# Kernel optimization log

Hardware: AMD Instinct MI355X
Metric: run time of the kernel (lower is better)

## Reference

```python
import jax, jax.numpy as jnp
import numpy as np

LAMBDA_MAX = 2.0  # standard re-scaled Laplacian assumption (DGL lambda_max=[2])
NUM_GRAPHS = 100


def _cheb(feat, src, dst, d_invsqrt, W, b):
    # DGL ChebConv: h = sum_i fc_i(X_i) + b, X_i = Chebyshev recursion on scaled Laplacian
    n = feat.shape[0]
    k = W.shape[0]
    re = 2.0 / LAMBDA_MAX

    def aggr(f):  # D^{-1/2} A D^{-1/2} f  via gather + segment_sum
        fh = f * d_invsqrt
        m = jax.ops.segment_sum(fh[src], dst, num_segments=n)
        return m * d_invsqrt

    X0 = feat
    h = X0 @ W[0]
    if k > 1:
        X1 = -re * aggr(X0) + X0 * (re - 1.0)
        h = h + X1 @ W[1]
        for i in range(2, k):
            Xi = -2.0 * re * aggr(X1) + X1 * (2.0 * (re - 1.0)) - X0
            h = h + Xi @ W[i]
            X0, X1 = X1, Xi
    return h + b


def _edgeconv(feat, src, dst, Wt, bt, Wp, bp):
    # DGL EdgeConv: out_i = max_{j->i} [theta(x_i - x_j) + phi(x_i)], 0 if no in-edges
    n = feat.shape[0]
    theta = (feat[dst] - feat[src]) @ Wt + bt           # [E, H]
    phi = feat @ Wp + bp                                # [N, H]
    msg = theta + phi[dst]                              # [E, H]
    agg = jax.ops.segment_max(msg, dst, num_segments=n)
    return jnp.where(jnp.isfinite(agg), agg, jnp.zeros((), feat.dtype))


def setup_inputs() -> dict:
    key = jax.random.key(0)
    ks = jax.random.split(key, 20)
    N, E, G = 100000, 1600000, NUM_GRAPHS
    IN, H, K = 16, 64, 3

    def lin(k, fan_in, shape):
        return jax.random.normal(k, shape, dtype=jnp.float32) * (1.0 / np.sqrt(fan_in))

    inp = {}
    inp["feat"] = jax.random.normal(ks[0], (N, IN), dtype=jnp.float32)
    inp["src"] = jax.random.randint(ks[1], (E,), 0, N)
    inp["dst"] = jax.random.randint(ks[2], (E,), 0, N)
    inp["graph_ids"] = jnp.sort(jax.random.randint(ks[3], (N,), 0, G))
    # ChebConv params: W [k, in, out], b [out]
    inp["W1"] = lin(ks[4], IN, (K, IN, H)); inp["b1"] = jnp.zeros((H,), jnp.float32)
    inp["W2"] = lin(ks[5], H, (K, H, H));   inp["b2"] = jnp.zeros((H,), jnp.float32)
    inp["W3"] = lin(ks[6], H, (K, H, H));   inp["b3"] = jnp.zeros((H,), jnp.float32)
    # EdgeConv params: theta + phi linears
    inp["Wt1"] = lin(ks[7], H, (H, H));  inp["bt1"] = jnp.zeros((H,), jnp.float32)
    inp["Wp1"] = lin(ks[8], H, (H, H));  inp["bp1"] = jnp.zeros((H,), jnp.float32)
    inp["Wt2"] = lin(ks[9], H, (H, H));  inp["bt2"] = jnp.zeros((H,), jnp.float32)
    inp["Wp2"] = lin(ks[10], H, (H, H)); inp["bp2"] = jnp.zeros((H,), jnp.float32)
    return inp


def reference(feat, src, dst, graph_ids, W1, b1, W2, b2, W3, b3,
              Wt1, bt1, Wp1, bp1, Wt2, bt2, Wp2, bp2):
    n = feat.shape[0]
    deg = jax.ops.segment_sum(jnp.ones((src.shape[0],), feat.dtype), dst, num_segments=n)
    d_invsqrt = (jnp.clip(deg, 1.0, None) ** -0.5)[:, None]  # [N, 1]

    h = jax.nn.relu(_cheb(feat, src, dst, d_invsqrt, W1, b1))
    h = jax.nn.relu(_edgeconv(h, src, dst, Wt1, bt1, Wp1, bp1))
    h = jax.nn.relu(_cheb(h, src, dst, d_invsqrt, W2, b2))
    h = jax.nn.relu(_edgeconv(h, src, dst, Wt2, bt2, Wp2, bp2))
    h = jax.nn.relu(_cheb(h, src, dst, d_invsqrt, W3, b3))

    # dgl.mean_nodes: per-graph mean pooling
    counts = jax.ops.segment_sum(jnp.ones((n,), h.dtype), graph_ids, num_segments=NUM_GRAPHS)
    hg = jax.ops.segment_sum(h, graph_ids, num_segments=NUM_GRAPHS)
    return hg / jnp.clip(counts, 1.0, None)[:, None]
```

## Files before the change

### kernel.cpp

```cpp
#include <hip/hip_runtime.h>
#include <hip/hip_bf16.h>
#include <math.h>

typedef __attribute__((ext_vector_type(8))) short short8;
typedef __attribute__((ext_vector_type(4))) float floatx4;

__device__ __forceinline__ unsigned short bfb(float x) {
    union { __hip_bfloat16 h; unsigned short u; } c;
    c.h = __float2bfloat16(x);
    return c.u;
}
__device__ __forceinline__ float bf2f(unsigned short u) {
    union { unsigned int i; float f; } c;
    c.i = ((unsigned int)u) << 16;
    return c.f;
}
__device__ __forceinline__ void acc2(float& lo, float& hi, unsigned d) {
    union { unsigned u; float f; } a, b;
    a.u = d << 16;
    b.u = d & 0xffff0000u;
    lo += a.f; hi += b.f;
}
__device__ __forceinline__ unsigned pkmaxu16(unsigned a, unsigned b) {
    unsigned d;
    asm("v_pk_max_u16 %0, %1, %2" : "=v"(d) : "v"(a), "v"(b));
    return d;
}


__global__ __launch_bounds__(256) void k_bhist(const int* __restrict__ dst, int* __restrict__ bcnt, int E) {
    __shared__ int h[512];
    int t = threadIdx.x;
    for (int i = t; i < 512; i += 256) h[i] = 0;
    __syncthreads();
    int step = gridDim.x * 256;
    for (int i = blockIdx.x * 256 + t; i < E; i += step) atomicAdd(&h[dst[i] >> 8], 1);
    __syncthreads();
    for (int i = t; i < 512; i += 256) if (h[i]) atomicAdd(&bcnt[i], h[i]);
}

__global__ __launch_bounds__(512) void k_scanBkt(const int* __restrict__ bcnt, int* __restrict__ boff,
                                                 int* __restrict__ bcur, int nb, int E) {
    __shared__ int s[512];
    int t = threadIdx.x;
    int v = (t < nb) ? bcnt[t] : 0;
    s[t] = v;
    __syncthreads();
    for (int off = 1; off < 512; off <<= 1) {
        int x = (t >= off) ? s[t - off] : 0;
        __syncthreads();
        s[t] += x;
        __syncthreads();
    }
    if (t < nb) { boff[t] = s[t] - v; bcur[t] = s[t] - v; }
    if (t == 0) boff[nb] = E;
}

#define PCHUNK 8192

__global__ __launch_bounds__(256) void k_partA(const int* __restrict__ src, const int* __restrict__ dst,
                                               int* __restrict__ bcur, unsigned* __restrict__ ebuf, int E) {
    __shared__ int h[512];
    __shared__ int base[512];
    int t = threadIdx.x;
    for (int i = t; i < 512; i += 256) h[i] = 0;
    __syncthreads();
    int start = blockIdx.x * PCHUNK;
    int end = start + PCHUNK < E ? start + PCHUNK : E;
    for (int i = start + t; i < end; i += 256) atomicAdd(&h[dst[i] >> 8], 1);
    __syncthreads();
    for (int i = t; i < 512; i += 256) {
        int c = h[i];
        base[i] = c ? atomicAdd(&bcur[i], c) : 0;
        h[i] = 0;
    }
    __syncthreads();
    for (int i = start + t; i < end; i += 256) {
        int d = dst[i];
        int b = d >> 8;
        int r = atomicAdd(&h[b], 1);
        ebuf[base[b] + r] = ((unsigned)src[i] << 8) | (unsigned)(d & 255);
    }
}

__global__ __launch_bounds__(256) void k_finish(const unsigned* __restrict__ ebuf, const int* __restrict__ boff,
                                                int* __restrict__ row_off, float* __restrict__ dinv,
                                                float* __restrict__ dsq, int* __restrict__ csr, int N, int E) {
    __shared__ int h[256];
    __shared__ int sc[256];
    __shared__ int cur[256];
    int b = blockIdx.x, t = threadIdx.x;
    h[t] = 0;
    __syncthreads();
    int beg = boff[b], end = boff[b + 1];
    for (int e = beg + t; e < end; e += 256) atomicAdd(&h[ebuf[e] & 255], 1);
    __syncthreads();
    int v = h[t];
    sc[t] = v;
    __syncthreads();
    for (int off = 1; off < 256; off <<= 1) {
        int x = (t >= off) ? sc[t - off] : 0;
        __syncthreads();
        sc[t] += x;
        __syncthreads();
    }
    int node = (b << 8) + t;
    int excl = beg + sc[t] - v;
    if (node < N) {
        row_off[node] = excl;
        float dg = (float)(v > 1 ? v : 1);
        dinv[node] = rsqrtf(dg);
        dsq[node] = sqrtf(dg);
    }
    cur[t] = excl;
    if (b == 0 && t == 0) row_off[N] = E;
    __syncthreads();
    for (int e = beg + t; e < end; e += 256) {
        unsigned ed = ebuf[e];
        int pos = atomicAdd(&cur[ed & 255], 1);
        csr[pos] = (int)(ed >> 8);
    }
}


__global__ __launch_bounds__(256) void k_feat16(const float* __restrict__ feat, const float* __restrict__ dinv,
                                                unsigned short* __restrict__ featd, int total) {
    int i = blockIdx.x * 256 + threadIdx.x;
    if (i < total) featd[i] = bfb(feat[i] * dinv[i >> 4]);
}


__global__ __launch_bounds__(256) void k_aggr16(const unsigned short* __restrict__ Xd, const float* __restrict__ Z,
                                                const float* __restrict__ dinv,
                                                const int* __restrict__ row_off, const int* __restrict__ csr,
                                                float* __restrict__ out, unsigned short* __restrict__ outd,
                                                float alpha, float beta, int zoff, int N) {
    int node = blockIdx.x * 4 + (threadIdx.x >> 6);
    if (node >= N) return;
    int lane = threadIdx.x & 63;
    int g = lane >> 2;
    int co = (lane & 3) * 8;
    int beg = row_off[node], end = row_off[node + 1];
    int deg = end - beg;
    int myOff = (lane < deg) ? (csr[beg + lane] << 5) : zoff;
    const char* base = (const char*)Xd + co;
    float a0 = 0.f, a1 = 0.f, a2 = 0.f, a3 = 0.f;
    {
        int o0 = __shfl(myOff, g);
        int o1 = __shfl(myOff, 16 + g);
        ushort4 x0 = *(const ushort4*)(base + o0);
        ushort4 x1 = *(const ushort4*)(base + o1);
        a0 += bf2f(x0.x); a1 += bf2f(x0.y); a2 += bf2f(x0.z); a3 += bf2f(x0.w);
        a0 += bf2f(x1.x); a1 += bf2f(x1.y); a2 += bf2f(x1.z); a3 += bf2f(x1.w);
    }
    if (deg > 32) {
        int dmain = deg < 64 ? deg : 64;
        for (int j = 32; j < dmain; j += 16) {
            int o = __shfl(myOff, j + g);
            ushort4 x = *(const ushort4*)(base + o);
            a0 += bf2f(x.x); a1 += bf2f(x.y); a2 += bf2f(x.z); a3 += bf2f(x.w);
        }
        for (int e = beg + 64; e < end; e += 16) {
            int idx = e + g;
            int s = csr[idx < end ? idx : end - 1];
            ushort4 x = *(const ushort4*)(base + (s << 5));
            if (idx < end) {
                a0 += bf2f(x.x); a1 += bf2f(x.y); a2 += bf2f(x.z); a3 += bf2f(x.w);
            }
        }
    }
    a0 += __shfl_xor(a0, 4); a0 += __shfl_xor(a0, 8); a0 += __shfl_xor(a0, 16); a0 += __shfl_xor(a0, 32);
    a1 += __shfl_xor(a1, 4); a1 += __shfl_xor(a1, 8); a1 += __shfl_xor(a1, 16); a1 += __shfl_xor(a1, 32);
    a2 += __shfl_xor(a2, 4); a2 += __shfl_xor(a2, 8); a2 += __shfl_xor(a2, 16); a2 += __shfl_xor(a2, 32);
    a3 += __shfl_xor(a3, 4); a3 += __shfl_xor(a3, 8); a3 += __shfl_xor(a3, 16); a3 += __shfl_xor(a3, 32);
    if (g == 0) {
        int c4 = (lane & 3) * 4;
        float dn = dinv[node];
        float v0 = alpha * dn * a0;
        float v1 = alpha * dn * a1;
        float v2 = alpha * dn * a2;
        float v3 = alpha * dn * a3;
        if (Z) {
            float4 zv = *(const float4*)&Z[(size_t)node * 16 + c4];
            v0 += beta * zv.x; v1 += beta * zv.y; v2 += beta * zv.z; v3 += beta * zv.w;
        }
        float4 r = { v0, v1, v2, v3 };
        *(float4*)&out[(size_t)node * 16 + c4] = r;
        if (outd) {
            ushort4 u = { bfb(v0 * dn), bfb(v1 * dn), bfb(v2 * dn), bfb(v3 * dn) };
            *(ushort4*)&outd[(size_t)node * 16 + c4] = u;
        }
    }
}


__global__ __launch_bounds__(256) void k_aggr64(const unsigned short* __restrict__ Xd,
                                                const unsigned short* __restrict__ Z,
                                                const float* __restrict__ dinv,
                                                const int* __restrict__ row_off, const int* __restrict__ csr,
                                                unsigned short* __restrict__ outb, unsigned short* __restrict__ outd,
                                                float alpha, float beta, int zoff, int N) {
    int node = blockIdx.x * 4 + (threadIdx.x >> 6);
    if (node >= N) return;
    int lane = threadIdx.x & 63;
    int g = lane >> 3;
    int co = (lane & 7) * 16;
    int beg = row_off[node], end = row_off[node + 1];
    int deg = end - beg;
    int myOff = (lane < deg) ? (csr[beg + lane] << 7) : zoff;
    const char* base = (const char*)Xd + co;
    float a0 = 0.f, a1 = 0.f, a2 = 0.f, a3 = 0.f, a4 = 0.f, a5 = 0.f, a6 = 0.f, a7 = 0.f;
    {
        int o0 = __shfl(myOff, g);
        int o1 = __shfl(myOff, 8 + g);
        int o2 = __shfl(myOff, 16 + g);
        int o3 = __shfl(myOff, 24 + g);
        uint4 x0 = *(const uint4*)(base + o0);
        uint4 x1 = *(const uint4*)(base + o1);
        uint4 x2 = *(const uint4*)(base + o2);
        uint4 x3 = *(const uint4*)(base + o3);
        acc2(a0, a1, x0.x); acc2(a2, a3, x0.y); acc2(a4, a5, x0.z); acc2(a6, a7, x0.w);
        acc2(a0, a1, x1.x); acc2(a2, a3, x1.y); acc2(a4, a5, x1.z); acc2(a6, a7, x1.w);
        acc2(a0, a1, x2.x); acc2(a2, a3, x2.y); acc2(a4, a5, x2.z); acc2(a6, a7, x2.w);
        acc2(a0, a1, x3.x); acc2(a2, a3, x3.y); acc2(a4, a5, x3.z); acc2(a6, a7, x3.w);
    }
    if (deg > 32) {
        int dmain = deg < 64 ? deg : 64;
        for (int j = 32; j < dmain; j += 8) {
            int o = __shfl(myOff, j + g);
            uint4 x = *(const uint4*)(base + o);
            acc2(a0, a1, x.x); acc2(a2, a3, x.y); acc2(a4, a5, x.z); acc2(a6, a7, x.w);
        }
        for (int e = beg + 64; e < end; e += 8) {
            int idx = e + g;
            int s = csr[idx < end ? idx : end - 1];
            uint4 x = *(const uint4*)(base + (s << 7));
            if (idx < end) {
                acc2(a0, a1, x.x); acc2(a2, a3, x.y); acc2(a4, a5, x.z); acc2(a6, a7, x.w);
            }
        }
    }
    a0 += __shfl_xor(a0, 8); a0 += __shfl_xor(a0, 16); a0 += __shfl_xor(a0, 32);
    a1 += __shfl_xor(a1, 8); a1 += __shfl_xor(a1, 16); a1 += __shfl_xor(a1, 32);
    a2 += __shfl_xor(a2, 8); a2 += __shfl_xor(a2, 16); a2 += __shfl_xor(a2, 32);
    a3 += __shfl_xor(a3, 8); a3 += __shfl_xor(a3, 16); a3 += __shfl_xor(a3, 32);
    a4 += __shfl_xor(a4, 8); a4 += __shfl_xor(a4, 16); a4 += __shfl_xor(a4, 32);
    a5 += __shfl_xor(a5, 8); a5 += __shfl_xor(a5, 16); a5 += __shfl_xor(a5, 32);
    a6 += __shfl_xor(a6, 8); a6 += __shfl_xor(a6, 16); a6 += __shfl_xor(a6, 32);
    a7 += __shfl_xor(a7, 8); a7 += __shfl_xor(a7, 16); a7 += __shfl_xor(a7, 32);
    if (g == 0) {
        float dn = dinv[node];
        float v[8] = { a0, a1, a2, a3, a4, a5, a6, a7 };
#pragma unroll
        for (int i = 0; i < 8; ++i) v[i] *= alpha * dn;
        size_t rb = (size_t)node * 128 + co;
        if (Z) {
            uint4 zv = *(const uint4*)((const char*)Z + rb);
            unsigned zd[4] = { zv.x, zv.y, zv.z, zv.w };
#pragma unroll
            for (int i = 0; i < 4; ++i) {
                union { unsigned u; float f; } lo, hi;
                lo.u = zd[i] << 16; hi.u = zd[i] & 0xffff0000u;
                v[2 * i] += beta * lo.f;
                v[2 * i + 1] += beta * hi.f;
            }
        }
        if (outb) {
            uint4 ub;
            unsigned* pb = (unsigned*)&ub;
#pragma unroll
            for (int i = 0; i < 4; ++i)
                pb[i] = (unsigned)bfb(v[2 * i]) | ((unsigned)bfb(v[2 * i + 1]) << 16);
            *(uint4*)((char*)outb + rb) = ub;
        }
        if (outd) {
            uint4 ud;
            unsigned* pd = (unsigned*)&ud;
#pragma unroll
            for (int i = 0; i < 4; ++i)
                pd[i] = (unsigned)bfb(v[2 * i] * dn) | ((unsigned)bfb(v[2 * i + 1] * dn) << 16);
            *(uint4*)((char*)outd + rb) = ud;
        }
    }
}


template <int KDIM, bool BIN16, bool FUSE_E1>
__global__ __launch_bounds__(256) void k_cheb(const void* __restrict__ X0v, const void* __restrict__ X1v,
                                              const void* __restrict__ X2v, const float* __restrict__ dsq,
                                              const float* __restrict__ W, const float* __restrict__ b,
                                              const float* __restrict__ Wt, const float* __restrict__ Wp,
                                              const float* __restrict__ bt, const float* __restrict__ bp,
                                              unsigned short* __restrict__ md, unsigned short* __restrict__ pbuf,
                                              float* __restrict__ outv, int N) {
    constexpr int KT = (KDIM == 16) ? 64 : 3 * KDIM;
    constexpr int SX = KT + 8;
    constexpr int PH1 = 2 * 64 * SX;
    constexpr int PH2 = FUSE_E1 ? (64 * 72 + 128 * 72) : 0;
    constexpr int SSZ = PH1 > PH2 ? PH1 : PH2;
    __shared__ unsigned short S[SSZ];
    unsigned short* Xs = S;
    unsigned short* Ws = S + 64 * SX;
    int t = threadIdx.x;

    {
        int sn = t & 63;
        int gn = blockIdx.x * 64 + sn; if (gn >= N) gn = N - 1;
        int k0 = (t >> 6) * (KDIM / 4);
        if constexpr (BIN16) {
            const unsigned short* Xp[3] = { (const unsigned short*)X0v, (const unsigned short*)X1v,
                                            (const unsigned short*)X2v };
#pragma unroll
            for (int a = 0; a < 3; ++a) {
#pragma unroll
                for (int i = 0; i < KDIM / 16; ++i) {
                    *(ushort4*)&Xs[sn * SX + a * KDIM + k0 + 4 * i] =
                        *(const ushort4*)&Xp[a][(size_t)gn * KDIM + k0 + 4 * i];
                }
            }
        } else {
            const float* Xp[3] = { (const float*)X0v, (const float*)X1v, (const float*)X2v };
#pragma unroll
            for (int a = 0; a < 3; ++a) {
#pragma unroll
                for (int i = 0; i < KDIM / 16; ++i) {
                    float4 v = *(const float4*)&Xp[a][(size_t)gn * KDIM + k0 + 4 * i];
                    ushort4 u = { bfb(v.x), bfb(v.y), bfb(v.z), bfb(v.w) };
                    *(ushort4*)&Xs[sn * SX + a * KDIM + k0 + 4 * i] = u;
                }
            }
        }
        if constexpr (KDIM == 16) {
            int kp = 48 + (t >> 6) * 4;
            ushort4 z = { 0, 0, 0, 0 };
            *(ushort4*)&Xs[sn * SX + kp] = z;
        }
    }
    for (int idx = t; idx < 3 * KDIM * 64; idx += 256) {
        int a = idx / (KDIM * 64);
        int r = idx % (KDIM * 64);
        int k = r >> 6, n = r & 63;
        Ws[n * SX + a * KDIM + k] = bfb(W[idx]);
    }
    if constexpr (KDIM == 16) {
        for (int idx = t; idx < 1024; idx += 256) {
            int n = idx & 63, k = 48 + (idx >> 6);
            Ws[n * SX + k] = 0;
        }
    }
    __syncthreads();

    int wave = t >> 6, lane = t & 63;
    int fi = lane & 15, quad = lane >> 4;
    int arow = wave * 16 + fi;

    floatx4 accA[4], accM[4];
#pragma unroll
    for (int i = 0; i < 4; ++i) { accA[i] = (floatx4){0.f,0.f,0.f,0.f}; accM[i] = (floatx4){0.f,0.f,0.f,0.f}; }
#pragma unroll
    for (int ks = 0; ks < KT / 32; ++ks) {
        constexpr bool hasMid = BIN16 && (KDIM == 64);
        short8 af = *(const short8*)&Xs[arow * SX + ks * 32 + quad * 8];
        short8 b0 = *(const short8*)&Ws[(0 * 16 + fi) * SX + ks * 32 + quad * 8];
        short8 b1 = *(const short8*)&Ws[(1 * 16 + fi) * SX + ks * 32 + quad * 8];
        short8 b2 = *(const short8*)&Ws[(2 * 16 + fi) * SX + ks * 32 + quad * 8];
        short8 b3 = *(const short8*)&Ws[(3 * 16 + fi) * SX + ks * 32 + quad * 8];
        if (hasMid && ks >= 2 && ks < 4) {
            accM[0] = __builtin_amdgcn_mfma_f32_16x16x32_bf16(af, b0, accM[0], 0, 0, 0);
            accM[1] = __builtin_amdgcn_mfma_f32_16x16x32_bf16(af, b1, accM[1], 0, 0, 0);
            accM[2] = __builtin_amdgcn_mfma_f32_16x16x32_bf16(af, b2, accM[2], 0, 0, 0);
            accM[3] = __builtin_amdgcn_mfma_f32_16x16x32_bf16(af, b3, accM[3], 0, 0, 0);
        } else {
            accA[0] = __builtin_amdgcn_mfma_f32_16x16x32_bf16(af, b0, accA[0], 0, 0, 0);
            accA[1] = __builtin_amdgcn_mfma_f32_16x16x32_bf16(af, b1, accA[1], 0, 0, 0);
            accA[2] = __builtin_amdgcn_mfma_f32_16x16x32_bf16(af, b2, accA[2], 0, 0, 0);
            accA[3] = __builtin_amdgcn_mfma_f32_16x16x32_bf16(af, b3, accA[3], 0, 0, 0);
        }
    }

    int nbase = blockIdx.x * 64 + wave * 16 + quad * 4;
    float dd[4];
#pragma unroll
    for (int reg = 0; reg < 4; ++reg) {
        if constexpr (BIN16 && KDIM == 64) {
            int node = nbase + reg;
            dd[reg] = dsq[node < N ? node : N - 1];
        } else dd[reg] = 0.f;
    }
    float rv[4][4];
#pragma unroll
    for (int nt = 0; nt < 4; ++nt) {
        int col = nt * 16 + fi;
        float bias = b[col];
#pragma unroll
        for (int reg = 0; reg < 4; ++reg) {
            float v = accA[nt][reg] + bias;
            if constexpr (BIN16 && KDIM == 64) v += accM[nt][reg] * dd[reg];
            rv[nt][reg] = fmaxf(v, 0.f);
        }
    }

    if constexpr (!FUSE_E1) {
#pragma unroll
        for (int nt = 0; nt < 4; ++nt) {
            int col = nt * 16 + fi;
#pragma unroll
            for (int reg = 0; reg < 4; ++reg) {
                int node = nbase + reg;
                if (node < N) outv[(size_t)node * 64 + col] = rv[nt][reg];
            }
        }
    } else {
        __syncthreads();
        unsigned short* Hs = S;
        unsigned short* W2 = S + 64 * 72;
        int lrow = wave * 16 + quad * 4;
#pragma unroll
        for (int nt = 0; nt < 4; ++nt) {
#pragma unroll
            for (int reg = 0; reg < 4; ++reg) {
                Hs[(lrow + reg) * 72 + nt * 16 + fi] = bfb(rv[nt][reg]);
            }
        }
        for (int idx = t; idx < 4096; idx += 256) {
            int k = idx >> 6, n = idx & 63;
            float wt = Wt[idx];
            W2[n * 72 + k] = bfb(wt);
            W2[(64 + n) * 72 + k] = bfb(wt + Wp[idx]);
        }
        __syncthreads();

        floatx4 ae[8];
#pragma unroll
        for (int i = 0; i < 8; ++i) ae[i] = (floatx4){0.f,0.f,0.f,0.f};
#pragma unroll
        for (int ks = 0; ks < 2; ++ks) {
            short8 af = *(const short8*)&Hs[arow * 72 + ks * 32 + quad * 8];
#pragma unroll
            for (int nt = 0; nt < 8; ++nt) {
                short8 bf = *(const short8*)&W2[(nt * 16 + fi) * 72 + ks * 32 + quad * 8];
                ae[nt] = __builtin_amdgcn_mfma_f32_16x16x32_bf16(af, bf, ae[nt], 0, 0, 0);
            }
        }
#pragma unroll
        for (int nt = 0; nt < 8; ++nt) {
            int col = nt * 16 + fi;
            if (col < 64) {
#pragma unroll
                for (int reg = 0; reg < 4; ++reg) {
                    int node = nbase + reg;
                    if (node < N) {
                        unsigned u = (unsigned)bfb(ae[nt][reg]) ^ 0x8000u;
                        unsigned key = (u & 0x8000u) ? (~u & 0xffffu) : (u | 0x8000u);
                        md[(size_t)node * 64 + col] = (unsigned short)key;
                    }
                }
            } else {
                int cc = col - 64;
                float bias = bt[cc] + bp[cc];
#pragma unroll
                for (int reg = 0; reg < 4; ++reg) {
                    int node = nbase + reg;
                    if (node < N) pbuf[(size_t)node * 64 + cc] = bfb(ae[nt][reg] + bias);
                }
            }
        }
    }
}


__global__ __launch_bounds__(256) void k_e2_b(const unsigned short* __restrict__ md,
                                              const unsigned short* __restrict__ pbuf,
                                              const int* __restrict__ row_off, const int* __restrict__ csr,
                                              const float* __restrict__ dinv, unsigned short* __restrict__ out,
                                              unsigned short* __restrict__ outd, int zoff, int N) {
    int node = blockIdx.x * 4 + (threadIdx.x >> 6);
    if (node >= N) return;
    int lane = threadIdx.x & 63;
    int g = lane >> 3;
    int co = (lane & 7) * 16;
    int beg = row_off[node], end = row_off[node + 1];
    int deg = end - beg;
    int dmain = deg < 64 ? deg : 64;
    int li = lane < dmain ? lane : dmain - 1;
    int myOff = (deg > 0) ? (csr[beg + li] << 7) : zoff;
    const char* base = (const char*)md + co;
    unsigned k0 = 0, k1 = 0, k2 = 0, k3 = 0;
    {
        int o0 = __shfl(myOff, g);
        int o1 = __shfl(myOff, 8 + g);
        int o2 = __shfl(myOff, 16 + g);
        int o3 = __shfl(myOff, 24 + g);
        uint4 x0 = *(const uint4*)(base + o0);
        uint4 x1 = *(const uint4*)(base + o1);
        uint4 x2 = *(const uint4*)(base + o2);
        uint4 x3 = *(const uint4*)(base + o3);
        k0 = pkmaxu16(k0, x0.x); k1 = pkmaxu16(k1, x0.y); k2 = pkmaxu16(k2, x0.z); k3 = pkmaxu16(k3, x0.w);
        k0 = pkmaxu16(k0, x1.x); k1 = pkmaxu16(k1, x1.y); k2 = pkmaxu16(k2, x1.z); k3 = pkmaxu16(k3, x1.w);
        k0 = pkmaxu16(k0, x2.x); k1 = pkmaxu16(k1, x2.y); k2 = pkmaxu16(k2, x2.z); k3 = pkmaxu16(k3, x2.w);
        k0 = pkmaxu16(k0, x3.x); k1 = pkmaxu16(k1, x3.y); k2 = pkmaxu16(k2, x3.z); k3 = pkmaxu16(k3, x3.w);
    }
    if (deg > 32) {
        for (int j = 32; j < dmain; j += 8) {
            int o = __shfl(myOff, j + g);
            uint4 x = *(const uint4*)(base + o);
            k0 = pkmaxu16(k0, x.x); k1 = pkmaxu16(k1, x.y); k2 = pkmaxu16(k2, x.z); k3 = pkmaxu16(k3, x.w);
        }
        for (int e = beg + 64; e < end; e += 8) {
            int idx = e + g;
            int s = csr[idx < end ? idx : end - 1];
            uint4 x = *(const uint4*)(base + (s << 7));
            k0 = pkmaxu16(k0, x.x); k1 = pkmaxu16(k1, x.y); k2 = pkmaxu16(k2, x.z); k3 = pkmaxu16(k3, x.w);
        }
    }
    k0 = pkmaxu16(k0, __shfl_xor((int)k0, 8)); k0 = pkmaxu16(k0, __shfl_xor((int)k0, 16)); k0 = pkmaxu16(k0, __shfl_xor((int)k0, 32));
    k1 = pkmaxu16(k1, __shfl_xor((int)k1, 8)); k1 = pkmaxu16(k1, __shfl_xor((int)k1, 16)); k1 = pkmaxu16(k1, __shfl_xor((int)k1, 32));
    k2 = pkmaxu16(k2, __shfl_xor((int)k2, 8)); k2 = pkmaxu16(k2, __shfl_xor((int)k2, 16)); k2 = pkmaxu16(k2, __shfl_xor((int)k2, 32));
    k3 = pkmaxu16(k3, __shfl_xor((int)k3, 8)); k3 = pkmaxu16(k3, __shfl_xor((int)k3, 16)); k3 = pkmaxu16(k3, __shfl_xor((int)k3, 32));
    if (g == 0) {
        unsigned kd[4] = { k0, k1, k2, k3 };
        float a[8];
#pragma unroll
        for (int i = 0; i < 4; ++i) {
            unsigned klo = kd[i] & 0xffffu, khi = kd[i] >> 16;
            unsigned short tlo = (klo & 0x8000u) ? (unsigned short)(klo & 0x7fffu) : (unsigned short)(~klo & 0xffffu);
            unsigned short thi = (khi & 0x8000u) ? (unsigned short)(khi & 0x7fffu) : (unsigned short)(~khi & 0xffffu);
            a[2 * i] = bf2f(tlo);
            a[2 * i + 1] = bf2f(thi);
        }
        float r[8];
        if (end > beg) {
            uint4 pk = *(const uint4*)((const char*)pbuf + (size_t)node * 128 + co);
            unsigned pd4[4] = { pk.x, pk.y, pk.z, pk.w };
#pragma unroll
            for (int i = 0; i < 4; ++i) {
                r[2 * i]     = fmaxf(bf2f((unsigned short)(pd4[i] & 0xffffu)) + a[2 * i], 0.f);
                r[2 * i + 1] = fmaxf(bf2f((unsigned short)(pd4[i] >> 16)) + a[2 * i + 1], 0.f);
            }
        } else {
#pragma unroll
            for (int i = 0; i < 8; ++i) r[i] = 0.f;
        }
        float dn = dinv[node];
        size_t rb = (size_t)node * 128 + co;
        uint4 ub, ud;
        unsigned* pb = (unsigned*)&ub;
        unsigned* pd = (unsigned*)&ud;
#pragma unroll
        for (int i = 0; i < 4; ++i) {
            pb[i] = (unsigned)bfb(r[2 * i]) | ((unsigned)bfb(r[2 * i + 1]) << 16);
            pd[i] = (unsigned)bfb(r[2 * i] * dn) | ((unsigned)bfb(r[2 * i + 1] * dn) << 16);
        }
        *(uint4*)((char*)out + rb) = ub;
        *(uint4*)((char*)outd + rb) = ud;
    }
}


__global__ __launch_bounds__(256) void k_pool(const float* __restrict__ h, const int* __restrict__ gid,
                                              float* __restrict__ out, float* __restrict__ gcnt, int N) {
    const int CHUNK = 128;
    int wave = blockIdx.x * 4 + (threadIdx.x >> 6);
    int lane = threadIdx.x & 63;
    int beg = wave * CHUNK;
    if (beg >= N) return;
    int end = beg + CHUNK < N ? beg + CHUNK : N;
    int gcur = gid[beg];
    float acc = 0.f;
    int cnt = 0;
    for (int n = beg; n < end; ++n) {
        int g = gid[n];
        float v = h[n * 64 + lane];
        if (g != gcur) {
            atomicAdd(&out[gcur * 64 + lane], acc);
            if (lane == 0) atomicAdd(&gcnt[gcur], (float)cnt);
            gcur = g; acc = 0.f; cnt = 0;
        }
        acc += v;
        ++cnt;
    }
    atomicAdd(&out[gcur * 64 + lane], acc);
    if (lane == 0) atomicAdd(&gcnt[gcur], (float)cnt);
}

__global__ __launch_bounds__(256) void k_div(float* __restrict__ out, const float* __restrict__ gcnt, int total) {
    int i = blockIdx.x * blockDim.x + threadIdx.x;
    if (i < total) out[i] /= fmaxf(gcnt[i >> 6], 1.f);
}


extern "C" void kernel_launch(void* const* d_in, const int* in_sizes, int n_in,
                              void* d_out, int out_size, void* d_ws, size_t ws_size,
                              hipStream_t stream) {
    const float* feat = (const float*)d_in[0];
    const int* src = (const int*)d_in[1];
    const int* dst = (const int*)d_in[2];
    const int* gid = (const int*)d_in[3];
    const float* W1 = (const float*)d_in[4];  const float* b1 = (const float*)d_in[5];
    const float* W2 = (const float*)d_in[6];  const float* b2 = (const float*)d_in[7];
    const float* W3 = (const float*)d_in[8];  const float* b3 = (const float*)d_in[9];
    const float* Wt1 = (const float*)d_in[10]; const float* bt1 = (const float*)d_in[11];
    const float* Wp1 = (const float*)d_in[12]; const float* bp1 = (const float*)d_in[13];
    const float* Wt2 = (const float*)d_in[14]; const float* bt2 = (const float*)d_in[15];
    const float* Wp2 = (const float*)d_in[16]; const float* bp2 = (const float*)d_in[17];
    float* out = (float*)d_out;

    const int N = in_sizes[0] / 16;
    const int E = in_sizes[1];
    const int G = out_size / 64;
    const int nb = (N + 255) >> 8;

    char* p = (char*)d_ws;
    auto alloc = [&](size_t nbytes) {
        void* r = (void*)p;
        p += (nbytes + 255) & ~(size_t)255;
        return r;
    };
    int* bcnt     = (int*)alloc(512 * 4);
    char* zpage   = (char*)alloc(256);
    float* gcnt   = (float*)alloc((size_t)G * 4);
    size_t zspan  = (size_t)((char*)gcnt - (char*)bcnt) + (((size_t)G * 4 + 255) & ~(size_t)255);
    int* boff     = (int*)alloc(513 * 4);
    int* bcur     = (int*)alloc(512 * 4);
    int* row_off  = (int*)alloc((size_t)(N + 1) * 4);
    int* csr      = (int*)alloc((size_t)E * 4);
    float* dinv   = (float*)alloc((size_t)N * 4);
    float* dsq    = (float*)alloc((size_t)N * 4);
    float* bufA   = (float*)alloc((size_t)N * 64 * 4);
    float* bufB   = (float*)alloc((size_t)N * 64 * 4);
    float* bufC   = (float*)alloc((size_t)N * 64 * 4);
    float* bufD   = (float*)alloc((size_t)N * 64 * 4);
    unsigned short* md   = (unsigned short*)alloc((size_t)N * 64 * 2);
    unsigned short* pbuf = (unsigned short*)alloc((size_t)N * 64 * 2);

    unsigned* ebuf = (unsigned*)bufA;
    unsigned short* hd = (unsigned short*)bufC;
    unsigned short* xd = hd + (size_t)N * 64;
    unsigned short* xd3 = (unsigned short*)bufA;
    unsigned short* hD = (unsigned short*)bufD;
    unsigned short* bufB16 = (unsigned short*)bufB;

    const int zo_hd = (int)((char*)zpage - (char*)hd);
    const int zo_xd = (int)((char*)zpage - (char*)xd);
    const int zo_xd3 = (int)((char*)zpage - (char*)xd3);
    const int zo_md = (int)((char*)zpage - (char*)md);

    hipMemsetAsync(bcnt, 0, zspan, stream);
    hipMemsetAsync(d_out, 0, (size_t)out_size * 4, stream);

    const int nb16 = (N * 16 + 255) / 256;
    const int nbw = (N + 3) / 4;
    const int npool = ((N + 127) / 128 + 3) / 4;
    const int nbt = (N + 63) / 64;
    const int npart = (E + PCHUNK - 1) / PCHUNK;

    k_bhist<<<256, 256, 0, stream>>>(dst, bcnt, E);
    k_scanBkt<<<1, 512, 0, stream>>>(bcnt, boff, bcur, nb, E);
    k_partA<<<npart, 256, 0, stream>>>(src, dst, bcur, ebuf, E);
    k_finish<<<nb, 256, 0, stream>>>(ebuf, boff, row_off, dinv, dsq, csr, N, E);

    k_feat16<<<nb16, 256, 0, stream>>>(feat, dinv, hd, N * 16);
    k_aggr16<<<nbw, 256, 0, stream>>>(hd, nullptr, dinv, row_off, csr, bufA, xd, -1.f, 0.f, zo_hd, N);
    k_aggr16<<<nbw, 256, 0, stream>>>(xd, feat, dinv, row_off, csr, bufB, nullptr, -2.f, -1.f, zo_xd, N);
    k_cheb<16, false, true><<<nbt, 256, 0, stream>>>(feat, bufA, bufB, nullptr, W1, b1,
                                                     Wt1, Wp1, bt1, bp1, md, pbuf, nullptr, N);
    k_e2_b<<<nbw, 256, 0, stream>>>(md, pbuf, row_off, csr, dinv, hD, hd, zo_md, N);

    k_aggr64<<<nbw, 256, 0, stream>>>(hd, nullptr, dinv, row_off, csr, nullptr, xd, -1.f, 0.f, zo_hd, N);
    k_aggr64<<<nbw, 256, 0, stream>>>(xd, hD, dinv, row_off, csr, bufB16, nullptr, -2.f, -1.f, zo_xd, N);
    k_cheb<64, true, true><<<nbt, 256, 0, stream>>>(hD, xd, bufB16, dsq, W2, b2,
                                                    Wt2, Wp2, bt2, bp2, md, pbuf, nullptr, N);
    k_e2_b<<<nbw, 256, 0, stream>>>(md, pbuf, row_off, csr, dinv, hD, hd, zo_md, N);

    k_aggr64<<<nbw, 256, 0, stream>>>(hd, nullptr, dinv, row_off, csr, nullptr, xd3, -1.f, 0.f, zo_hd, N);
    k_aggr64<<<nbw, 256, 0, stream>>>(xd3, hD, dinv, row_off, csr, bufB16, nullptr, -2.f, -1.f, zo_xd3, N);
    k_cheb<64, true, false><<<nbt, 256, 0, stream>>>(hD, xd3, bufB16, dsq, W3, b3,
                                                     nullptr, nullptr, nullptr, nullptr,
                                                     nullptr, nullptr, bufC, N);

    k_pool<<<npool, 256, 0, stream>>>(bufC, gid, out, gcnt, N);
    k_div<<<(out_size + 255) / 256, 256, 0, stream>>>(out, gcnt, out_size);
}
```

Measured before the change: 568.3 us.

## Fuse feature scaling into CSR finish, pooling into last Cheb, bf16 aggr16 outputs

Folds the feat-to-bf16 scaling into k_finish, which removes a separate kernel launch. The final Cheb layer now adds straight into the per-graph output with atomics, using a wave-level reduction when all 16 rows belong to one graph. This drops the fp32 N×64 intermediate write and the separate pool kernel. k_aggr16 now writes bf16 instead of fp32, halving that traffic, and k_div gets the per-graph node counts by binary search over the sorted graph ids. The costs are more atomic contention on the output and extra precision loss from the bf16 intermediates.

```diff
diff --git a/kernel.cpp b/kernel.cpp
--- a/kernel.cpp
+++ b/kernel.cpp
@@ -85,7 +85,9 @@
 
 __global__ __launch_bounds__(256) void k_finish(const unsigned* __restrict__ ebuf, const int* __restrict__ boff,
                                                 int* __restrict__ row_off, float* __restrict__ dinv,
-                                                float* __restrict__ dsq, int* __restrict__ csr, int N, int E) {
+                                                float* __restrict__ dsq, int* __restrict__ csr,
+                                                const float* __restrict__ feat, unsigned short* __restrict__ hd,
+                                                int N, int E) {
     __shared__ int h[256];
     __shared__ int sc[256];
     __shared__ int cur[256];
@@ -109,8 +111,16 @@
     if (node < N) {
         row_off[node] = excl;
         float dg = (float)(v > 1 ? v : 1);
-        dinv[node] = rsqrtf(dg);
+        float dv = rsqrtf(dg);
+        dinv[node] = dv;
         dsq[node] = sqrtf(dg);
+        const float* f = &feat[(size_t)node * 16];
+#pragma unroll
+        for (int k = 0; k < 16; k += 4) {
+            float4 x = *(const float4*)&f[k];
+            ushort4 u = { bfb(x.x * dv), bfb(x.y * dv), bfb(x.z * dv), bfb(x.w * dv) };
+            *(ushort4*)&hd[(size_t)node * 16 + k] = u;
+        }
     }
     cur[t] = excl;
     if (b == 0 && t == 0) row_off[N] = E;
@@ -123,17 +133,10 @@
 }
 
 
-__global__ __launch_bounds__(256) void k_feat16(const float* __restrict__ feat, const float* __restrict__ dinv,
-                                                unsigned short* __restrict__ featd, int total) {
-    int i = blockIdx.x * 256 + threadIdx.x;
-    if (i < total) featd[i] = bfb(feat[i] * dinv[i >> 4]);
-}
-
-
 __global__ __launch_bounds__(256) void k_aggr16(const unsigned short* __restrict__ Xd, const float* __restrict__ Z,
                                                 const float* __restrict__ dinv,
                                                 const int* __restrict__ row_off, const int* __restrict__ csr,
-                                                float* __restrict__ out, unsigned short* __restrict__ outd,
+                                                unsigned short* __restrict__ outb, unsigned short* __restrict__ outd,
                                                 float alpha, float beta, int zoff, int N) {
     int node = blockIdx.x * 4 + (threadIdx.x >> 6);
     if (node >= N) return;
@@ -184,8 +187,8 @@
             float4 zv = *(const float4*)&Z[(size_t)node * 16 + c4];
             v0 += beta * zv.x; v1 += beta * zv.y; v2 += beta * zv.z; v3 += beta * zv.w;
         }
-        float4 r = { v0, v1, v2, v3 };
-        *(float4*)&out[(size_t)node * 16 + c4] = r;
+        ushort4 ub = { bfb(v0), bfb(v1), bfb(v2), bfb(v3) };
+        *(ushort4*)&outb[(size_t)node * 16 + c4] = ub;
         if (outd) {
             ushort4 u = { bfb(v0 * dn), bfb(v1 * dn), bfb(v2 * dn), bfb(v3 * dn) };
             *(ushort4*)&outd[(size_t)node * 16 + c4] = u;
@@ -285,19 +288,20 @@
 }
 
 
-template <int KDIM, bool BIN16, bool FUSE_E1>
+template <int KDIM, bool FUSE_E1, bool POOLOUT>
 __global__ __launch_bounds__(256) void k_cheb(const void* __restrict__ X0v, const void* __restrict__ X1v,
                                               const void* __restrict__ X2v, const float* __restrict__ dsq,
-                                              const float* __restrict__ W, const float* __restrict__ b,
+                                              const float* __restrict__ W, const float* __restrict__ bvec,
                                               const float* __restrict__ Wt, const float* __restrict__ Wp,
                                               const float* __restrict__ bt, const float* __restrict__ bp,
                                               unsigned short* __restrict__ md, unsigned short* __restrict__ pbuf,
-                                              float* __restrict__ outv, int N) {
+                                              const int* __restrict__ gid, float* __restrict__ out, int N) {
     constexpr int KT = (KDIM == 16) ? 64 : 3 * KDIM;
     constexpr int SX = KT + 8;
     constexpr int PH1 = 2 * 64 * SX;
     constexpr int PH2 = FUSE_E1 ? (64 * 72 + 128 * 72) : 0;
     constexpr int SSZ = PH1 > PH2 ? PH1 : PH2;
+    constexpr bool hasMid = (KDIM == 64);
     __shared__ unsigned short S[SSZ];
     unsigned short* Xs = S;
     unsigned short* Ws = S + 64 * SX;
@@ -307,7 +311,18 @@
         int sn = t & 63;
         int gn = blockIdx.x * 64 + sn; if (gn >= N) gn = N - 1;
         int k0 = (t >> 6) * (KDIM / 4);
-        if constexpr (BIN16) {
+        if constexpr (KDIM == 16) {
+            float4 v = *(const float4*)&((const float*)X0v)[(size_t)gn * 16 + k0];
+            ushort4 u = { bfb(v.x), bfb(v.y), bfb(v.z), bfb(v.w) };
+            *(ushort4*)&Xs[sn * SX + k0] = u;
+            *(ushort4*)&Xs[sn * SX + 16 + k0] =
+                *(const ushort4*)&((const unsigned short*)X1v)[(size_t)gn * 16 + k0];
+            *(ushort4*)&Xs[sn * SX + 32 + k0] =
+                *(const ushort4*)&((const unsigned short*)X2v)[(size_t)gn * 16 + k0];
+            int kp = 48 + (t >> 6) * 4;
+            ushort4 z = { 0, 0, 0, 0 };
+            *(ushort4*)&Xs[sn * SX + kp] = z;
+        } else {
             const unsigned short* Xp[3] = { (const unsigned short*)X0v, (const unsigned short*)X1v,
                                             (const unsigned short*)X2v };
 #pragma unroll
@@ -318,22 +333,6 @@
                         *(const ushort4*)&Xp[a][(size_t)gn * KDIM + k0 + 4 * i];
                 }
             }
-        } else {
-            const float* Xp[3] = { (const float*)X0v, (const float*)X1v, (const float*)X2v };
-#pragma unroll
-            for (int a = 0; a < 3; ++a) {
-#pragma unroll
-                for (int i = 0; i < KDIM / 16; ++i) {
-                    float4 v = *(const float4*)&Xp[a][(size_t)gn * KDIM + k0 + 4 * i];
-                    ushort4 u = { bfb(v.x), bfb(v.y), bfb(v.z), bfb(v.w) };
-                    *(ushort4*)&Xs[sn * SX + a * KDIM + k0 + 4 * i] = u;
-                }
-            }
-        }
-        if constexpr (KDIM == 16) {
-            int kp = 48 + (t >> 6) * 4;
-            ushort4 z = { 0, 0, 0, 0 };
-            *(ushort4*)&Xs[sn * SX + kp] = z;
         }
     }
     for (int idx = t; idx < 3 * KDIM * 64; idx += 256) {
@@ -359,7 +358,6 @@
     for (int i = 0; i < 4; ++i) { accA[i] = (floatx4){0.f,0.f,0.f,0.f}; accM[i] = (floatx4){0.f,0.f,0.f,0.f}; }
 #pragma unroll
     for (int ks = 0; ks < KT / 32; ++ks) {
-        constexpr bool hasMid = BIN16 && (KDIM == 64);
         short8 af = *(const short8*)&Xs[arow * SX + ks * 32 + quad * 8];
         short8 b0 = *(const short8*)&Ws[(0 * 16 + fi) * SX + ks * 32 + quad * 8];
         short8 b1 = *(const short8*)&Ws[(1 * 16 + fi) * SX + ks * 32 + quad * 8];
@@ -378,11 +376,12 @@
         }
     }
 
-    int nbase = blockIdx.x * 64 + wave * 16 + quad * 4;
+    int nbase0 = blockIdx.x * 64 + wave * 16;
+    int nbase = nbase0 + quad * 4;
     float dd[4];
 #pragma unroll
     for (int reg = 0; reg < 4; ++reg) {
-        if constexpr (BIN16 && KDIM == 64) {
+        if constexpr (hasMid) {
             int node = nbase + reg;
             dd[reg] = dsq[node < N ? node : N - 1];
         } else dd[reg] = 0.f;
@@ -391,45 +390,56 @@
 #pragma unroll
     for (int nt = 0; nt < 4; ++nt) {
         int col = nt * 16 + fi;
-        float bias = b[col];
+        float bias = bvec[col];
 #pragma unroll
         for (int reg = 0; reg < 4; ++reg) {
             float v = accA[nt][reg] + bias;
-            if constexpr (BIN16 && KDIM == 64) v += accM[nt][reg] * dd[reg];
+            if constexpr (hasMid) v += accM[nt][reg] * dd[reg];
             rv[nt][reg] = fmaxf(v, 0.f);
         }
     }
 
-    if constexpr (!FUSE_E1) {
-#pragma unroll
-        for (int nt = 0; nt < 4; ++nt) {
-            int col = nt * 16 + fi;
+    if constexpr (POOLOUT) {
+        int gfirst = gid[nbase0 < N ? nbase0 : N - 1];
+        int lastn = nbase0 + 15;
+        int glast = gid[lastn < N ? lastn : N - 1];
+        bool uniform = (lastn < N) && (gfirst == glast);
+        if (uniform) {
+#pragma unroll
+            for (int nt = 0; nt < 4; ++nt) {
+                float s = (rv[nt][0] + rv[nt][1]) + (rv[nt][2] + rv[nt][3]);
+                s += __shfl_xor(s, 16); s += __shfl_xor(s, 32);
+                if (quad == 0) atomicAdd(&out[(size_t)gfirst * 64 + nt * 16 + fi], s);
+            }
+        } else {
 #pragma unroll
             for (int reg = 0; reg < 4; ++reg) {
                 int node = nbase + reg;
-                if (node < N) outv[(size_t)node * 64 + col] = rv[nt][reg];
-            }
-        }
-    } else {
+                if (node < N) {
+                    int g = gid[node];
+#pragma unroll
+                    for (int nt = 0; nt < 4; ++nt)
+                        atomicAdd(&out[(size_t)g * 64 + nt * 16 + fi], rv[nt][reg]);
+                }
+            }
+        }
+    } else if constexpr (FUSE_E1) {
         __syncthreads();
         unsigned short* Hs = S;
-        unsigned short* W2 = S + 64 * 72;
+        unsigned short* W2l = S + 64 * 72;
         int lrow = wave * 16 + quad * 4;
 #pragma unroll
-        for (int nt = 0; nt < 4; ++nt) {
-#pragma unroll
-            for (int reg = 0; reg < 4; ++reg) {
+        for (int nt = 0; nt < 4; ++nt)
+#pragma unroll
+            for (int reg = 0; reg < 4; ++reg)
                 Hs[(lrow + reg) * 72 + nt * 16 + fi] = bfb(rv[nt][reg]);
-            }
-        }
         for (int idx = t; idx < 4096; idx += 256) {
             int k = idx >> 6, n = idx & 63;
             float wt = Wt[idx];
-            W2[n * 72 + k] = bfb(wt);
-            W2[(64 + n) * 72 + k] = bfb(wt + Wp[idx]);
+            W2l[n * 72 + k] = bfb(wt);
+            W2l[(64 + n) * 72 + k] = bfb(wt + Wp[idx]);
         }
         __syncthreads();
-
         floatx4 ae[8];
 #pragma unroll
         for (int i = 0; i < 8; ++i) ae[i] = (floatx4){0.f,0.f,0.f,0.f};
@@ -438,7 +448,7 @@
             short8 af = *(const short8*)&Hs[arow * 72 + ks * 32 + quad * 8];
 #pragma unroll
             for (int nt = 0; nt < 8; ++nt) {
-                short8 bf = *(const short8*)&W2[(nt * 16 + fi) * 72 + ks * 32 + quad * 8];
+                short8 bf = *(const short8*)&W2l[(nt * 16 + fi) * 72 + ks * 32 + quad * 8];
                 ae[nt] = __builtin_amdgcn_mfma_f32_16x16x32_bf16(af, bf, ae[nt], 0, 0, 0);
             }
         }
@@ -457,11 +467,11 @@
                 }
             } else {
                 int cc = col - 64;
-                float bias = bt[cc] + bp[cc];
+                float bias2 = bt[cc] + bp[cc];
 #pragma unroll
                 for (int reg = 0; reg < 4; ++reg) {
                     int node = nbase + reg;
-                    if (node < N) pbuf[(size_t)node * 64 + cc] = bfb(ae[nt][reg] + bias);
+                    if (node < N) pbuf[(size_t)node * 64 + cc] = bfb(ae[nt][reg] + bias2);
                 }
             }
         }
@@ -557,35 +567,18 @@
 }
 
 
-__global__ __launch_bounds__(256) void k_pool(const float* __restrict__ h, const int* __restrict__ gid,
-                                              float* __restrict__ out, float* __restrict__ gcnt, int N) {
-    const int CHUNK = 128;
-    int wave = blockIdx.x * 4 + (threadIdx.x >> 6);
-    int lane = threadIdx.x & 63;
-    int beg = wave * CHUNK;
-    if (beg >= N) return;
-    int end = beg + CHUNK < N ? beg + CHUNK : N;
-    int gcur = gid[beg];
-    float acc = 0.f;
-    int cnt = 0;
-    for (int n = beg; n < end; ++n) {
-        int g = gid[n];
-        float v = h[n * 64 + lane];
-        if (g != gcur) {
-            atomicAdd(&out[gcur * 64 + lane], acc);
-            if (lane == 0) atomicAdd(&gcnt[gcur], (float)cnt);
-            gcur = g; acc = 0.f; cnt = 0;
-        }
-        acc += v;
-        ++cnt;
-    }
-    atomicAdd(&out[gcur * 64 + lane], acc);
-    if (lane == 0) atomicAdd(&gcnt[gcur], (float)cnt);
-}
-
-__global__ __launch_bounds__(256) void k_div(float* __restrict__ out, const float* __restrict__ gcnt, int total) {
+__global__ __launch_bounds__(256) void k_div(float* __restrict__ out, const int* __restrict__ gid,
+                                             int N, int total) {
     int i = blockIdx.x * blockDim.x + threadIdx.x;
-    if (i < total) out[i] /= fmaxf(gcnt[i >> 6], 1.f);
+    if (i >= total) return;
+    int g = i >> 6;
+    int lo = 0, hi = N;
+    while (lo < hi) { int m = (lo + hi) >> 1; if (gid[m] < g) lo = m + 1; else hi = m; }
+    int s = lo;
+    hi = N;
+    while (lo < hi) { int m = (lo + hi) >> 1; if (gid[m] < g + 1) lo = m + 1; else hi = m; }
+    float c = (float)(lo - s);
+    out[i] /= fmaxf(c, 1.f);
 }
 
 
@@ -607,7 +600,6 @@
 
     const int N = in_sizes[0] / 16;
     const int E = in_sizes[1];
-    const int G = out_size / 64;
     const int nb = (N + 255) >> 8;
 
     char* p = (char*)d_ws;
@@ -618,8 +610,7 @@
     };
     int* bcnt     = (int*)alloc(512 * 4);
     char* zpage   = (char*)alloc(256);
-    float* gcnt   = (float*)alloc((size_t)G * 4);
-    size_t zspan  = (size_t)((char*)gcnt - (char*)bcnt) + (((size_t)G * 4 + 255) & ~(size_t)255);
+    size_t zspan  = (size_t)((char*)zpage - (char*)bcnt) + 256;
     int* boff     = (int*)alloc(513 * 4);
     int* bcur     = (int*)alloc(512 * 4);
     int* row_off  = (int*)alloc((size_t)(N + 1) * 4);
@@ -636,9 +627,10 @@
     unsigned* ebuf = (unsigned*)bufA;
     unsigned short* hd = (unsigned short*)bufC;
     unsigned short* xd = hd + (size_t)N * 64;
+    unsigned short* xA16 = (unsigned short*)bufA;
+    unsigned short* xB16 = (unsigned short*)bufB;
     unsigned short* xd3 = (unsigned short*)bufA;
     unsigned short* hD = (unsigned short*)bufD;
-    unsigned short* bufB16 = (unsigned short*)bufB;
 
     const int zo_hd = (int)((char*)zpage - (char*)hd);
     const int zo_xd = (int)((char*)zpage - (char*)xd);
@@ -648,36 +640,32 @@
     hipMemsetAsync(bcnt, 0, zspan, stream);
     hipMemsetAsync(d_out, 0, (size_t)out_size * 4, stream);
 
-    const int nb16 = (N * 16 + 255) / 256;
     const int nbw = (N + 3) / 4;
-    const int npool = ((N + 127) / 128 + 3) / 4;
     const int nbt = (N + 63) / 64;
     const int npart = (E + PCHUNK - 1) / PCHUNK;
 
     k_bhist<<<256, 256, 0, stream>>>(dst, bcnt, E);
     k_scanBkt<<<1, 512, 0, stream>>>(bcnt, boff, bcur, nb, E);
     k_partA<<<npart, 256, 0, stream>>>(src, dst, bcur, ebuf, E);
-    k_finish<<<nb, 256, 0, stream>>>(ebuf, boff, row_off, dinv, dsq, csr, N, E);
-
-    k_feat16<<<nb16, 256, 0, stream>>>(feat, dinv, hd, N * 16);
-    k_aggr16<<<nbw, 256, 0, stream>>>(hd, nullptr, dinv, row_off, csr, bufA, xd, -1.f, 0.f, zo_hd, N);
-    k_aggr16<<<nbw, 256, 0, stream>>>(xd, feat, dinv, row_off, csr, bufB, nullptr, -2.f, -1.f, zo_xd, N);
-    k_cheb<16, false, true><<<nbt, 256, 0, stream>>>(feat, bufA, bufB, nullptr, W1, b1,
-                                                     Wt1, Wp1, bt1, bp1, md, pbuf, nullptr, N);
+    k_finish<<<nb, 256, 0, stream>>>(ebuf, boff, row_off, dinv, dsq, csr, feat, hd, N, E);
+
+    k_aggr16<<<nbw, 256, 0, stream>>>(hd, nullptr, dinv, row_off, csr, xA16, xd, -1.f, 0.f, zo_hd, N);
+    k_aggr16<<<nbw, 256, 0, stream>>>(xd, feat, dinv, row_off, csr, xB16, nullptr, -2.f, -1.f, zo_xd, N);
+    k_cheb<16, true, false><<<nbt, 256, 0, stream>>>(feat, xA16, xB16, nullptr, W1, b1,
+                                                     Wt1, Wp1, bt1, bp1, md, pbuf, nullptr, nullptr, N);
     k_e2_b<<<nbw, 256, 0, stream>>>(md, pbuf, row_off, csr, dinv, hD, hd, zo_md, N);
 
     k_aggr64<<<nbw, 256, 0, stream>>>(hd, nullptr, dinv, row_off, csr, nullptr, xd, -1.f, 0.f, zo_hd, N);
-    k_aggr64<<<nbw, 256, 0, stream>>>(xd, hD, dinv, row_off, csr, bufB16, nullptr, -2.f, -1.f, zo_xd, N);
-    k_cheb<64, true, true><<<nbt, 256, 0, stream>>>(hD, xd, bufB16, dsq, W2, b2,
-                                                    Wt2, Wp2, bt2, bp2, md, pbuf, nullptr, N);
+    k_aggr64<<<nbw, 256, 0, stream>>>(xd, hD, dinv, row_off, csr, xB16, nullptr, -2.f, -1.f, zo_xd, N);
+    k_cheb<64, true, false><<<nbt, 256, 0, stream>>>(hD, xd, xB16, dsq, W2, b2,
+                                                     Wt2, Wp2, bt2, bp2, md, pbuf, nullptr, nullptr, N);
     k_e2_b<<<nbw, 256, 0, stream>>>(md, pbuf, row_off, csr, dinv, hD, hd, zo_md, N);
 
     k_aggr64<<<nbw, 256, 0, stream>>>(hd, nullptr, dinv, row_off, csr, nullptr, xd3, -1.f, 0.f, zo_hd, N);
-    k_aggr64<<<nbw, 256, 0, stream>>>(xd3, hD, dinv, row_off, csr, bufB16, nullptr, -2.f, -1.f, zo_xd3, N);
-    k_cheb<64, true, false><<<nbt, 256, 0, stream>>>(hD, xd3, bufB16, dsq, W3, b3,
+    k_aggr64<<<nbw, 256, 0, stream>>>(xd3, hD, dinv, row_off, csr, xB16, nullptr, -2.f, -1.f, zo_xd3, N);
+    k_cheb<64, false, true><<<nbt, 256, 0, stream>>>(hD, xd3, xB16, dsq, W3, b3,
                                                      nullptr, nullptr, nullptr, nullptr,
-                                                     nullptr, nullptr, bufC, N);
-
-    k_pool<<<npool, 256, 0, stream>>>(bufC, gid, out, gcnt, N);
-    k_div<<<(out_size + 255) / 256, 256, 0, stream>>>(out, gcnt, out_size);
-}
+                                                     nullptr, nullptr, gid, out, N);
+
+    k_div<<<(out_size + 255) / 256, 256, 0, stream>>>(out, gid, N, out_size);
+}
```

Measured after the change: 533.7 us. -6.1%, faster.
